# Kernel optimization log

Measured on AMD Instinct MI355X. Metric: run time of the kernel, lower is better.

Reference implementation:

```python
import jax, jax.numpy as jnp
import numpy as np

B, T, I, H, O = 64, 512, 256, 512, 256

def setup_inputs() -> dict:
    key = jax.random.key(0)
    ks = jax.random.split(key, 12)
    s = 1.0 / np.sqrt(H)
    u = lambda k, shp: jax.random.uniform(k, shp, jnp.float32, -s, s)
    return {
        'x': jax.random.normal(ks[0], (B, T, I), jnp.float32),
        'w_ih0': u(ks[1], (H, I)),  'w_hh0': u(ks[2], (H, H)),
        'b_ih0': u(ks[3], (H,)),    'b_hh0': u(ks[4], (H,)),
        'w_ih1': u(ks[5], (H, H)),  'w_hh1': u(ks[6], (H, H)),
        'b_ih1': u(ks[7], (H,)),    'b_hh1': u(ks[8], (H,)),
        'fc_w': u(ks[9], (O, H)),   'fc_b': u(ks[10], (O,)),
    }

def _rnn_layer(inp, w_ih, w_hh, b_ih, b_hh):
    # inp: [B, T, F] -> precompute input projection once (one big GEMM)
    xp = jnp.einsum('btf,hf->bth', inp, w_ih) + b_ih + b_hh  # [B, T, H]
    def step(h, xt):
        h = jnp.tanh(xt + h @ w_hh.T)  # [B, H]
        return h, h
    h0 = jnp.zeros((inp.shape[0], w_hh.shape[0]), inp.dtype)
    hT, outs = jax.lax.scan(step, h0, jnp.swapaxes(xp, 0, 1))  # outs: [T, B, H]
    return jnp.swapaxes(outs, 0, 1), hT

def reference(x, w_ih0, w_hh0, b_ih0, b_hh0, w_ih1, w_hh1, b_ih1, b_hh1, fc_w, fc_b):
    out0, h0f = _rnn_layer(x, w_ih0, w_hh0, b_ih0, b_hh0)
    out1, h1f = _rnn_layer(out0, w_ih1, w_hh1, b_ih1, b_hh1)
    hidden = jnp.stack([h0f, h1f])                  # [n_layers, B, H]
    out = out1.reshape(-1, out1.shape[-1]) @ fc_w.T + fc_b  # [B*T, O]
    return out, hidden
```

## Files before the change

### kernel.cpp

```cpp
#include <hip/hip_runtime.h>

#define B_  64
#define T_  512
#define I_  256
#define H_  512
#define O_  256
#define SENT 0x7F7F7F7Fu
#define SLOT_BYTES 8192u

typedef __attribute__((ext_vector_type(8))) __bf16 bf16x8;
typedef __attribute__((ext_vector_type(4))) float f32x4;
typedef unsigned int u32x4 __attribute__((ext_vector_type(4)));

__device__ __forceinline__ unsigned short f2bf(float f) {
    unsigned int u = __float_as_uint(f);
    unsigned int r = (u + 0x7fffu + ((u >> 16) & 1u)) >> 16;
    return (unsigned short)r;
}

__device__ __forceinline__ float tanh_fast(float x) {
    float e = __expf(2.0f * x);
    float d = e + 1.0f;
    float r;
    asm("v_rcp_f32 %0, %1" : "=v"(r) : "v"(d));
    return 1.0f - 2.0f * r;
}

__global__ void cvt_kernel(const float* __restrict__ in, unsigned short* __restrict__ out, int n4) {
    int i = blockIdx.x * blockDim.x + threadIdx.x;
    if (i >= n4) return;
    float4 f = reinterpret_cast<const float4*>(in)[i];
    ushort4 o;
    o.x = f2bf(f.x); o.y = f2bf(f.y); o.z = f2bf(f.z); o.w = f2bf(f.w);
    reinterpret_cast<ushort4*>(out)[i] = o;
}

__global__ __launch_bounds__(256) void gemm_kernel(
    const unsigned short* __restrict__ A,
    const unsigned short* __restrict__ Bw,
    const float* __restrict__ b0,
    const float* __restrict__ b1,
    float* __restrict__ C,
    int M, int N, int K, int perm)
{
    const int m0 = blockIdx.x * 64;
    const int n0 = blockIdx.y * 64;
    const int tid = threadIdx.x;
    const int wv = tid >> 6;
    const int l = tid & 63;
    const int lr = l & 15;
    const int lk = (l >> 4) * 8;
    const int arow = m0 + wv * 16 + lr;

    f32x4 acc[4] = {{0,0,0,0},{0,0,0,0},{0,0,0,0},{0,0,0,0}};
    const int nks = K / 32;
    for (int ks = 0; ks < nks; ++ks) {
        bf16x8 a = *reinterpret_cast<const bf16x8*>(A + (size_t)arow * K + ks * 32 + lk);
        #pragma unroll
        for (int nt = 0; nt < 4; ++nt) {
            bf16x8 b = *reinterpret_cast<const bf16x8*>(Bw + (size_t)(n0 + nt * 16 + lr) * K + ks * 32 + lk);
            acc[nt] = __builtin_amdgcn_mfma_f32_16x16x32_bf16(a, b, acc[nt], 0, 0, 0);
        }
    }
    #pragma unroll
    for (int nt = 0; nt < 4; ++nt) {
        #pragma unroll
        for (int r = 0; r < 4; ++r) {
            int row = m0 + wv * 16 + (l >> 4) * 4 + r;
            int col = n0 + nt * 16 + lr;
            float v = acc[nt][r];
            if (b0) v += b0[col];
            if (b1) v += b1[col];
            int cs = perm ? ((col & 15) * 32 + (col >> 4)) : col;
            C[(size_t)row * N + cs] = v;
        }
    }
}

#define LDW8(ARR, BASE) \
    asm volatile( \
        "global_load_dwordx4 %0, %8, %9 offset:0\n\t" \
        "global_load_dwordx4 %1, %8, %9 offset:64\n\t" \
        "global_load_dwordx4 %2, %8, %9 offset:128\n\t" \
        "global_load_dwordx4 %3, %8, %9 offset:192\n\t" \
        "global_load_dwordx4 %4, %8, %9 offset:256\n\t" \
        "global_load_dwordx4 %5, %8, %9 offset:320\n\t" \
        "global_load_dwordx4 %6, %8, %9 offset:384\n\t" \
        "global_load_dwordx4 %7, %8, %9 offset:448\n\t" \
        "s_waitcnt vmcnt(0)" \
        : "=&v"(ARR[0]), "=&v"(ARR[1]), "=&v"(ARR[2]), "=&v"(ARR[3]), \
          "=&v"(ARR[4]), "=&v"(ARR[5]), "=&v"(ARR[6]), "=&v"(ARR[7]) \
        : "v"(BASE), "s"(w))

#define LOAD_XP4(XPQ) \
    asm volatile( \
        "global_load_dwordx4 %0, %4, %8\n\t" \
        "global_load_dwordx4 %1, %5, %8\n\t" \
        "global_load_dwordx4 %2, %6, %8\n\t" \
        "global_load_dwordx4 %3, %7, %8\n\t" \
        "s_waitcnt vmcnt(0)" \
        : "=&v"(XPQ[0]), "=&v"(XPQ[1]), "=&v"(XPQ[2]), "=&v"(XPQ[3]) \
        : "v"(vxpr[0]), "v"(vxpr[1]), "v"(vxpr[2]), "v"(vxpr[3]), "s"(xpg))

#define ISSUE_XP4(XPQ) \
    asm volatile( \
        "global_load_dwordx4 %0, %4, %8\n\t" \
        "global_load_dwordx4 %1, %5, %8\n\t" \
        "global_load_dwordx4 %2, %6, %8\n\t" \
        "global_load_dwordx4 %3, %7, %8" \
        : "=&v"(XPQ[0]), "=&v"(XPQ[1]), "=&v"(XPQ[2]), "=&v"(XPQ[3]) \
        : "v"(vxpr[0]), "v"(vxpr[1]), "v"(vxpr[2]), "v"(vxpr[3]), "s"(xpg))

#define POLL8(AFP, VSLR, SC) \
    asm volatile( \
        "global_load_dwordx4 %0, %8, %9 " SC "\n\t" \
        "global_load_dwordx4 %1, %8, %9 offset:64 " SC "\n\t" \
        "global_load_dwordx4 %2, %8, %9 offset:128 " SC "\n\t" \
        "global_load_dwordx4 %3, %8, %9 offset:192 " SC "\n\t" \
        "global_load_dwordx4 %4, %8, %9 offset:256 " SC "\n\t" \
        "global_load_dwordx4 %5, %8, %9 offset:320 " SC "\n\t" \
        "global_load_dwordx4 %6, %8, %9 offset:384 " SC "\n\t" \
        "global_load_dwordx4 %7, %8, %9 offset:448 " SC "\n\t" \
        "s_waitcnt vmcnt(0)" \
        : "=&v"(AFP[0]), "=&v"(AFP[1]), "=&v"(AFP[2]), "=&v"(AFP[3]), \
          "=&v"(AFP[4]), "=&v"(AFP[5]), "=&v"(AFP[6]), "=&v"(AFP[7]) \
        : "v"(VSLR), "s"(slR))

#define SENT_CHECK(AFP, BAD) \
    { BAD = 0; \
      _Pragma("unroll") \
      for (int _i = 0; _i < 8; ++_i) \
          _Pragma("unroll") \
          for (int _j = 0; _j < 4; ++_j) \
              BAD |= (AFP[_i][_j] == SENT); }

#define STORE_SLOT16(PK, VSLW) \
    asm volatile( \
        "global_store_dword %16, %0, %17 sc0 sc1\n\t" \
        "global_store_dword %16, %1, %17 offset:512 sc0 sc1\n\t" \
        "global_store_dword %16, %2, %17 offset:1024 sc0 sc1\n\t" \
        "global_store_dword %16, %3, %17 offset:1536 sc0 sc1\n\t" \
        "global_store_dword %16, %4, %17 offset:32 sc0 sc1\n\t" \
        "global_store_dword %16, %5, %17 offset:544 sc0 sc1\n\t" \
        "global_store_dword %16, %6, %17 offset:1056 sc0 sc1\n\t" \
        "global_store_dword %16, %7, %17 offset:1568 sc0 sc1\n\t" \
        "global_store_dword %16, %8, %17 offset:64 sc0 sc1\n\t" \
        "global_store_dword %16, %9, %17 offset:576 sc0 sc1\n\t" \
        "global_store_dword %16, %10, %17 offset:1088 sc0 sc1\n\t" \
        "global_store_dword %16, %11, %17 offset:1600 sc0 sc1\n\t" \
        "global_store_dword %16, %12, %17 offset:96 sc0 sc1\n\t" \
        "global_store_dword %16, %13, %17 offset:608 sc0 sc1\n\t" \
        "global_store_dword %16, %14, %17 offset:1120 sc0 sc1\n\t" \
        "global_store_dword %16, %15, %17 offset:1632 sc0 sc1" \
        :: "v"(PK[0]), "v"(PK[1]), "v"(PK[2]), "v"(PK[3]), \
           "v"(PK[4]), "v"(PK[5]), "v"(PK[6]), "v"(PK[7]), \
           "v"(PK[8]), "v"(PK[9]), "v"(PK[10]), "v"(PK[11]), \
           "v"(PK[12]), "v"(PK[13]), "v"(PK[14]), "v"(PK[15]), \
           "v"(VSLW), "s"(slW) \
        : "memory")

#define OUT16(PK) \
    asm volatile( \
        "global_store_dword %16, %0, %20\n\t" \
        "global_store_dword %17, %1, %20\n\t" \
        "global_store_dword %18, %2, %20\n\t" \
        "global_store_dword %19, %3, %20\n\t" \
        "global_store_dword %16, %4, %20 offset:32\n\t" \
        "global_store_dword %17, %5, %20 offset:32\n\t" \
        "global_store_dword %18, %6, %20 offset:32\n\t" \
        "global_store_dword %19, %7, %20 offset:32\n\t" \
        "global_store_dword %16, %8, %20 offset:64\n\t" \
        "global_store_dword %17, %9, %20 offset:64\n\t" \
        "global_store_dword %18, %10, %20 offset:64\n\t" \
        "global_store_dword %19, %11, %20 offset:64\n\t" \
        "global_store_dword %16, %12, %20 offset:96\n\t" \
        "global_store_dword %17, %13, %20 offset:96\n\t" \
        "global_store_dword %18, %14, %20 offset:96\n\t" \
        "global_store_dword %19, %15, %20 offset:96" \
        :: "v"(PK[0]), "v"(PK[1]), "v"(PK[2]), "v"(PK[3]), \
           "v"(PK[4]), "v"(PK[5]), "v"(PK[6]), "v"(PK[7]), \
           "v"(PK[8]), "v"(PK[9]), "v"(PK[10]), "v"(PK[11]), \
           "v"(PK[12]), "v"(PK[13]), "v"(PK[14]), "v"(PK[15]), \
           "v"(vout[0]), "v"(vout[1]), "v"(vout[2]), "v"(vout[3]), \
           "s"(out_bf) \
        : "memory")

#define SENTRESET(VS) \
    asm volatile( \
        "global_store_dwordx4 %0, %1, %2 sc0 sc1\n\t" \
        "global_store_dwordx4 %0, %1, %2 offset:1024 sc0 sc1" \
        :: "v"(VS), "v"(sentq), "s"(slR) : "memory")

__global__ __launch_bounds__(256, 1) void recur_kernel(
    const float* __restrict__ xp,
    const unsigned short* __restrict__ w,
    unsigned short* __restrict__ out_bf,
    float* __restrict__ h_final,
    unsigned short* __restrict__ slots)
{
    __shared__ __align__(16) unsigned short lds[16 * 280];

    const int bid16 = blockIdx.x;
    if (bid16 & 4) return;
    const int g   = bid16 & 3;
    const int jw  = (bid16 >> 3) & 1;
    const int widx = g * 2 + jw;
    const int pjw = jw ^ 1;
    const int b0  = g * 16;
    const int tid = threadIdx.x;
    const int wv  = tid >> 6;
    const int l   = tid & 63;
    const int lr  = l & 15;
    const int lk  = (l >> 4) * 8;
    const int jn0 = jw * 256 + wv * 64;
    const int erow_l = (l >> 4) * 4;
    const int erow_g = b0 + erow_l;

    const float*          xpg = xp + (size_t)b0 * T_ * H_;
    float*                hfg = h_final + (size_t)b0 * H_;
    unsigned short*       slW = slots + (size_t)widx * 16384;
    const unsigned short* slR = slots + (size_t)(widx ^ 1) * 16384;

    bf16x8 bwo[4][8], bwp[4][8];
    #pragma unroll
    for (int nt = 0; nt < 4; ++nt) {
        unsigned int vo = (unsigned)((jn0 + nt * 16 + lr) * (H_ * 2) + jw  * 512 + lk * 2);
        unsigned int vp = (unsigned)((jn0 + nt * 16 + lr) * (H_ * 2) + pjw * 512 + lk * 2);
        LDW8(bwo[nt], vo);
        LDW8(bwp[nt], vp);
    }

    unsigned int vxpr[4], vout[4];
    #pragma unroll
    for (int r = 0; r < 4; ++r) {
        vxpr[r] = (unsigned)(((erow_l + r) * T_ * H_ + lr * 32 + jw * 16 + wv * 4) * 4);
        vout[r] = (unsigned)(((erow_g + r) * T_) * H_ * 2 + (jn0 + lr) * 2);
    }
    const unsigned int vslr0 = (unsigned)(lr * 512 + lk * 2);
    const unsigned int vslw0 = (unsigned)(erow_l * 512 + (wv * 64 + lr) * 2);
    const unsigned int vsent0 = (unsigned)(wv * 2048 + l * 16);
    const u32x4 sentq = {SENT, SENT, SENT, SENT};
    const int cb = wv * 32 + (lr >> 1);

    unsigned int pks[16];
    f32x4 xpq[4];

    {
        LOAD_XP4(xpq);
        #pragma unroll
        for (int nt = 0; nt < 4; ++nt)
            #pragma unroll
            for (int r = 0; r < 4; ++r) {
                float hv = tanh_fast(xpq[r][nt]);
                unsigned int mine = f2bf(hv);
                unsigned int oth = (unsigned int)__shfl_xor((int)mine, 1, 64);
                pks[nt * 4 + r] = mine | (oth << 16);
            }
        if (!(lr & 1)) {
            unsigned int* lw = (unsigned int*)lds;
            #pragma unroll
            for (int nt = 0; nt < 4; ++nt)
                #pragma unroll
                for (int r = 0; r < 4; ++r)
                    lw[(erow_l + r) * 140 + cb + nt * 8] = pks[nt * 4 + r];
            unsigned int vslw = vslw0 + 1u * SLOT_BYTES;
            STORE_SLOT16(pks, vslw);
        }
        #pragma unroll
        for (int r = 0; r < 4; ++r) vxpr[r] += H_ * 4;
        ISSUE_XP4(xpq);
        __syncthreads();
    }

    for (int t = 1; t < T_; ++t) {
        f32x4 acc[4] = {{0,0,0,0},{0,0,0,0},{0,0,0,0},{0,0,0,0}};
        {
            bf16x8 afo[8];
            const unsigned short* lrb = lds + lr * 280 + lk;
            #pragma unroll
            for (int i = 0; i < 8; ++i)
                afo[i] = *reinterpret_cast<const bf16x8*>(lrb + i * 32);
            #pragma unroll
            for (int i = 0; i < 8; ++i) {
                acc[0] = __builtin_amdgcn_mfma_f32_16x16x32_bf16(afo[i], bwo[0][i], acc[0], 0, 0, 0);
                acc[1] = __builtin_amdgcn_mfma_f32_16x16x32_bf16(afo[i], bwo[1][i], acc[1], 0, 0, 0);
                acc[2] = __builtin_amdgcn_mfma_f32_16x16x32_bf16(afo[i], bwo[2][i], acc[2], 0, 0, 0);
                acc[3] = __builtin_amdgcn_mfma_f32_16x16x32_bf16(afo[i], bwo[3][i], acc[3], 0, 0, 0);
            }
        }
        __syncthreads();

        const unsigned int vslr = vslr0 + (unsigned)(t & 3) * SLOT_BYTES;
        u32x4 afp[8];
        int bad;
        POLL8(afp, vslr, "sc0");
        SENT_CHECK(afp, bad);
        while (__any(bad)) {
            POLL8(afp, vslr, "sc0 sc1");
            SENT_CHECK(afp, bad);
            if (!__any(bad)) break;
            POLL8(afp, vslr, "sc0");
            SENT_CHECK(afp, bad);
        }
        __builtin_amdgcn_sched_barrier(0);

        if (!(lr & 1)) OUT16(pks);
        #pragma unroll
        for (int r = 0; r < 4; ++r) vout[r] += H_ * 2;

        #pragma unroll
        for (int i = 0; i < 8; ++i) {
            bf16x8 a = __builtin_bit_cast(bf16x8, afp[i]);
            acc[0] = __builtin_amdgcn_mfma_f32_16x16x32_bf16(a, bwp[0][i], acc[0], 0, 0, 0);
            acc[1] = __builtin_amdgcn_mfma_f32_16x16x32_bf16(a, bwp[1][i], acc[1], 0, 0, 0);
            acc[2] = __builtin_amdgcn_mfma_f32_16x16x32_bf16(a, bwp[2][i], acc[2], 0, 0, 0);
            acc[3] = __builtin_amdgcn_mfma_f32_16x16x32_bf16(a, bwp[3][i], acc[3], 0, 0, 0);
        }

        unsigned int pkn[16];
        #pragma unroll
        for (int nt = 0; nt < 4; ++nt)
            #pragma unroll
            for (int r = 0; r < 4; ++r) {
                float pre = acc[nt][r] + xpq[r][nt];
                float hv = tanh_fast(pre);
                if (t == T_ - 1)
                    hfg[(size_t)(erow_l + r) * H_ + jn0 + nt * 16 + lr] = hv;
                unsigned int mine = f2bf(hv);
                unsigned int oth = (unsigned int)__shfl_xor((int)mine, 1, 64);
                pkn[nt * 4 + r] = mine | (oth << 16);
            }
        if (!(lr & 1)) {
            unsigned int* lw = (unsigned int*)lds;
            #pragma unroll
            for (int nt = 0; nt < 4; ++nt)
                #pragma unroll
                for (int r = 0; r < 4; ++r)
                    lw[(erow_l + r) * 140 + cb + nt * 8] = pkn[nt * 4 + r];
            unsigned int vslw = vslw0 + (unsigned)((t + 1) & 3) * SLOT_BYTES;
            STORE_SLOT16(pkn, vslw);
        }
        #pragma unroll
        for (int r = 0; r < 4; ++r) vxpr[r] += H_ * 4;
        if (t < T_ - 1) ISSUE_XP4(xpq);
        #pragma unroll
        for (int i = 0; i < 16; ++i) pks[i] = pkn[i];

        __syncthreads();
        {
            unsigned int vs = vsent0 + (unsigned)(t & 3) * SLOT_BYTES;
            SENTRESET(vs);
        }
    }

    if (!(lr & 1)) OUT16(pks);
}

#define OFF_XBF    ((size_t)0)
#define OFF_WIH0   ((size_t)16777216)
#define OFF_WHH0   ((size_t)17039360)
#define OFF_WIH1   ((size_t)17563648)
#define OFF_WHH1   ((size_t)18087936)
#define OFF_FCW    ((size_t)18612224)
#define OFF_XP     ((size_t)18874368)
#define OFF_OUTBF  ((size_t)85983232)
#define OFF_SLOTS  ((size_t)119537664)
#define WS_NEED    ((size_t)119799808)

extern "C" void kernel_launch(void* const* d_in, const int* in_sizes, int n_in,
                              void* d_out, int out_size, void* d_ws, size_t ws_size,
                              hipStream_t stream) {
    if (ws_size < WS_NEED) return;
    const float* x     = (const float*)d_in[0];
    const float* w_ih0 = (const float*)d_in[1];
    const float* w_hh0 = (const float*)d_in[2];
    const float* b_ih0 = (const float*)d_in[3];
    const float* b_hh0 = (const float*)d_in[4];
    const float* w_ih1 = (const float*)d_in[5];
    const float* w_hh1 = (const float*)d_in[6];
    const float* b_ih1 = (const float*)d_in[7];
    const float* b_hh1 = (const float*)d_in[8];
    const float* fc_w  = (const float*)d_in[9];
    const float* fc_b  = (const float*)d_in[10];

    char* ws = (char*)d_ws;
    unsigned short* x_bf     = (unsigned short*)(ws + OFF_XBF);
    unsigned short* w_ih0_bf = (unsigned short*)(ws + OFF_WIH0);
    unsigned short* w_hh0_bf = (unsigned short*)(ws + OFF_WHH0);
    unsigned short* w_ih1_bf = (unsigned short*)(ws + OFF_WIH1);
    unsigned short* w_hh1_bf = (unsigned short*)(ws + OFF_WHH1);
    unsigned short* fc_w_bf  = (unsigned short*)(ws + OFF_FCW);
    float*          xp       = (float*)(ws + OFF_XP);
    unsigned short* out_bf   = (unsigned short*)(ws + OFF_OUTBF);
    unsigned short* slots    = (unsigned short*)(ws + OFF_SLOTS);

    float* out  = (float*)d_out;
    float* hid0 = out + (size_t)B_ * T_ * O_;
    float* hid1 = hid0 + (size_t)B_ * H_;

    hipMemsetAsync(ws + OFF_SLOTS, 0x7F, 262144, stream);

    auto cvt = [&](const float* in, unsigned short* o, int n) {
        int n4 = n / 4;
        cvt_kernel<<<(n4 + 255) / 256, 256, 0, stream>>>(in, o, n4);
    };
    cvt(x,     x_bf,     B_ * T_ * I_);
    cvt(w_ih0, w_ih0_bf, H_ * I_);
    cvt(w_hh0, w_hh0_bf, H_ * H_);
    cvt(w_ih1, w_ih1_bf, H_ * H_);
    cvt(w_hh1, w_hh1_bf, H_ * H_);
    cvt(fc_w,  fc_w_bf,  O_ * H_);

    const int M = B_ * T_;

    gemm_kernel<<<dim3(M / 64, H_ / 64), 256, 0, stream>>>(
        x_bf, w_ih0_bf, b_ih0, b_hh0, xp, M, H_, I_, 1);

    recur_kernel<<<16, 256, 0, stream>>>(xp, w_hh0_bf, out_bf, hid0, slots);

    gemm_kernel<<<dim3(M / 64, H_ / 64), 256, 0, stream>>>(
        out_bf, w_ih1_bf, b_ih1, b_hh1, xp, M, H_, H_, 1);

    hipMemsetAsync(ws + OFF_SLOTS, 0x7F, 262144, stream);

    recur_kernel<<<16, 256, 0, stream>>>(xp, w_hh1_bf, out_bf, hid1, slots);

    gemm_kernel<<<dim3(M / 64, O_ / 64), 256, 0, stream>>>(
        out_bf, fc_w_bf, fc_b, nullptr, out, M, O_, H_, 0);
}
```

Baseline: 4.307 ms.

## Process two batch groups per recurrent workgroup, halving workgroup count

Result: slower. 7.233 ms (+67.9%).

```diff
diff --git a/kernel.cpp b/kernel.cpp
--- a/kernel.cpp
+++ b/kernel.cpp
@@ -92,7 +92,7 @@
           "=&v"(ARR[4]), "=&v"(ARR[5]), "=&v"(ARR[6]), "=&v"(ARR[7]) \
         : "v"(BASE), "s"(w))
 
-#define LOAD_XP4(XPQ) \
+#define LOAD_XP4(XPQ, XPB) \
     asm volatile( \
         "global_load_dwordx4 %0, %4, %8\n\t" \
         "global_load_dwordx4 %1, %5, %8\n\t" \
@@ -100,41 +100,79 @@
         "global_load_dwordx4 %3, %7, %8\n\t" \
         "s_waitcnt vmcnt(0)" \
         : "=&v"(XPQ[0]), "=&v"(XPQ[1]), "=&v"(XPQ[2]), "=&v"(XPQ[3]) \
-        : "v"(vxpr[0]), "v"(vxpr[1]), "v"(vxpr[2]), "v"(vxpr[3]), "s"(xpg))
-
-#define ISSUE_XP4(XPQ) \
-    asm volatile( \
-        "global_load_dwordx4 %0, %4, %8\n\t" \
-        "global_load_dwordx4 %1, %5, %8\n\t" \
-        "global_load_dwordx4 %2, %6, %8\n\t" \
-        "global_load_dwordx4 %3, %7, %8" \
-        : "=&v"(XPQ[0]), "=&v"(XPQ[1]), "=&v"(XPQ[2]), "=&v"(XPQ[3]) \
-        : "v"(vxpr[0]), "v"(vxpr[1]), "v"(vxpr[2]), "v"(vxpr[3]), "s"(xpg))
-
-#define POLL8(AFP, VSLR, SC) \
-    asm volatile( \
-        "global_load_dwordx4 %0, %8, %9 " SC "\n\t" \
-        "global_load_dwordx4 %1, %8, %9 offset:64 " SC "\n\t" \
-        "global_load_dwordx4 %2, %8, %9 offset:128 " SC "\n\t" \
-        "global_load_dwordx4 %3, %8, %9 offset:192 " SC "\n\t" \
-        "global_load_dwordx4 %4, %8, %9 offset:256 " SC "\n\t" \
-        "global_load_dwordx4 %5, %8, %9 offset:320 " SC "\n\t" \
-        "global_load_dwordx4 %6, %8, %9 offset:384 " SC "\n\t" \
-        "global_load_dwordx4 %7, %8, %9 offset:448 " SC "\n\t" \
+        : "v"(vxpr[0]), "v"(vxpr[1]), "v"(vxpr[2]), "v"(vxpr[3]), "s"(XPB))
+
+#define LOAD2_XP_PEER() \
+    asm volatile( \
+        "global_load_dwordx4 %0, %24, %28\n\t" \
+        "global_load_dwordx4 %1, %25, %28\n\t" \
+        "global_load_dwordx4 %2, %26, %28\n\t" \
+        "global_load_dwordx4 %3, %27, %28\n\t" \
+        "global_load_dwordx4 %4, %24, %29\n\t" \
+        "global_load_dwordx4 %5, %25, %29\n\t" \
+        "global_load_dwordx4 %6, %26, %29\n\t" \
+        "global_load_dwordx4 %7, %27, %29\n\t" \
+        "global_load_dwordx4 %8, %30, %31 sc0 sc1\n\t" \
+        "global_load_dwordx4 %9, %30, %31 offset:64 sc0 sc1\n\t" \
+        "global_load_dwordx4 %10, %30, %31 offset:128 sc0 sc1\n\t" \
+        "global_load_dwordx4 %11, %30, %31 offset:192 sc0 sc1\n\t" \
+        "global_load_dwordx4 %12, %30, %31 offset:256 sc0 sc1\n\t" \
+        "global_load_dwordx4 %13, %30, %31 offset:320 sc0 sc1\n\t" \
+        "global_load_dwordx4 %14, %30, %31 offset:384 sc0 sc1\n\t" \
+        "global_load_dwordx4 %15, %30, %31 offset:448 sc0 sc1\n\t" \
+        "global_load_dwordx4 %16, %30, %32 sc0 sc1\n\t" \
+        "global_load_dwordx4 %17, %30, %32 offset:64 sc0 sc1\n\t" \
+        "global_load_dwordx4 %18, %30, %32 offset:128 sc0 sc1\n\t" \
+        "global_load_dwordx4 %19, %30, %32 offset:192 sc0 sc1\n\t" \
+        "global_load_dwordx4 %20, %30, %32 offset:256 sc0 sc1\n\t" \
+        "global_load_dwordx4 %21, %30, %32 offset:320 sc0 sc1\n\t" \
+        "global_load_dwordx4 %22, %30, %32 offset:384 sc0 sc1\n\t" \
+        "global_load_dwordx4 %23, %30, %32 offset:448 sc0 sc1\n\t" \
         "s_waitcnt vmcnt(0)" \
-        : "=&v"(AFP[0]), "=&v"(AFP[1]), "=&v"(AFP[2]), "=&v"(AFP[3]), \
-          "=&v"(AFP[4]), "=&v"(AFP[5]), "=&v"(AFP[6]), "=&v"(AFP[7]) \
-        : "v"(VSLR), "s"(slR))
-
-#define SENT_CHECK(AFP, BAD) \
+        : "=&v"(xpqA[0]), "=&v"(xpqA[1]), "=&v"(xpqA[2]), "=&v"(xpqA[3]), \
+          "=&v"(xpqB[0]), "=&v"(xpqB[1]), "=&v"(xpqB[2]), "=&v"(xpqB[3]), \
+          "=&v"(afpA[0]), "=&v"(afpA[1]), "=&v"(afpA[2]), "=&v"(afpA[3]), \
+          "=&v"(afpA[4]), "=&v"(afpA[5]), "=&v"(afpA[6]), "=&v"(afpA[7]), \
+          "=&v"(afpB[0]), "=&v"(afpB[1]), "=&v"(afpB[2]), "=&v"(afpB[3]), \
+          "=&v"(afpB[4]), "=&v"(afpB[5]), "=&v"(afpB[6]), "=&v"(afpB[7]) \
+        : "v"(vxpr[0]), "v"(vxpr[1]), "v"(vxpr[2]), "v"(vxpr[3]), \
+          "s"(xpA), "s"(xpB), "v"(vslr), "s"(slRA), "s"(slRB))
+
+#define RETRY16() \
+    asm volatile( \
+        "global_load_dwordx4 %0, %16, %17 sc0 sc1\n\t" \
+        "global_load_dwordx4 %1, %16, %17 offset:64 sc0 sc1\n\t" \
+        "global_load_dwordx4 %2, %16, %17 offset:128 sc0 sc1\n\t" \
+        "global_load_dwordx4 %3, %16, %17 offset:192 sc0 sc1\n\t" \
+        "global_load_dwordx4 %4, %16, %17 offset:256 sc0 sc1\n\t" \
+        "global_load_dwordx4 %5, %16, %17 offset:320 sc0 sc1\n\t" \
+        "global_load_dwordx4 %6, %16, %17 offset:384 sc0 sc1\n\t" \
+        "global_load_dwordx4 %7, %16, %17 offset:448 sc0 sc1\n\t" \
+        "global_load_dwordx4 %8, %16, %18 sc0 sc1\n\t" \
+        "global_load_dwordx4 %9, %16, %18 offset:64 sc0 sc1\n\t" \
+        "global_load_dwordx4 %10, %16, %18 offset:128 sc0 sc1\n\t" \
+        "global_load_dwordx4 %11, %16, %18 offset:192 sc0 sc1\n\t" \
+        "global_load_dwordx4 %12, %16, %18 offset:256 sc0 sc1\n\t" \
+        "global_load_dwordx4 %13, %16, %18 offset:320 sc0 sc1\n\t" \
+        "global_load_dwordx4 %14, %16, %18 offset:384 sc0 sc1\n\t" \
+        "global_load_dwordx4 %15, %16, %18 offset:448 sc0 sc1\n\t" \
+        "s_waitcnt vmcnt(0)" \
+        : "=&v"(afpA[0]), "=&v"(afpA[1]), "=&v"(afpA[2]), "=&v"(afpA[3]), \
+          "=&v"(afpA[4]), "=&v"(afpA[5]), "=&v"(afpA[6]), "=&v"(afpA[7]), \
+          "=&v"(afpB[0]), "=&v"(afpB[1]), "=&v"(afpB[2]), "=&v"(afpB[3]), \
+          "=&v"(afpB[4]), "=&v"(afpB[5]), "=&v"(afpB[6]), "=&v"(afpB[7]) \
+        : "v"(vslr), "s"(slRA), "s"(slRB))
+
+#define SENT_CHECK2(BAD) \
     { BAD = 0; \
       _Pragma("unroll") \
       for (int _i = 0; _i < 8; ++_i) \
           _Pragma("unroll") \
-          for (int _j = 0; _j < 4; ++_j) \
-              BAD |= (AFP[_i][_j] == SENT); }
-
-#define STORE_SLOT16(PK, VSLW) \
+          for (int _j = 0; _j < 4; ++_j) { \
+              BAD |= (afpA[_i][_j] == SENT); \
+              BAD |= (afpB[_i][_j] == SENT); } }
+
+#define STORE_SLOT16(PK, VSLW, SLWB) \
     asm volatile( \
         "global_store_dword %16, %0, %17 sc0 sc1\n\t" \
         "global_store_dword %16, %1, %17 offset:512 sc0 sc1\n\t" \
@@ -156,10 +194,10 @@
            "v"(PK[4]), "v"(PK[5]), "v"(PK[6]), "v"(PK[7]), \
            "v"(PK[8]), "v"(PK[9]), "v"(PK[10]), "v"(PK[11]), \
            "v"(PK[12]), "v"(PK[13]), "v"(PK[14]), "v"(PK[15]), \
-           "v"(VSLW), "s"(slW) \
+           "v"(VSLW), "s"(SLWB) \
         : "memory")
 
-#define OUT16(PK) \
+#define OUT16(PK, OUTB) \
     asm volatile( \
         "global_store_dword %16, %0, %20\n\t" \
         "global_store_dword %17, %1, %20\n\t" \
@@ -182,14 +220,14 @@
            "v"(PK[8]), "v"(PK[9]), "v"(PK[10]), "v"(PK[11]), \
            "v"(PK[12]), "v"(PK[13]), "v"(PK[14]), "v"(PK[15]), \
            "v"(vout[0]), "v"(vout[1]), "v"(vout[2]), "v"(vout[3]), \
-           "s"(out_bf) \
+           "s"(OUTB) \
         : "memory")
 
-#define SENTRESET(VS) \
+#define SENTRESET(VS, SLRB) \
     asm volatile( \
         "global_store_dwordx4 %0, %1, %2 sc0 sc1\n\t" \
         "global_store_dwordx4 %0, %1, %2 offset:1024 sc0 sc1" \
-        :: "v"(VS), "v"(sentq), "s"(slR) : "memory")
+        :: "v"(VS), "v"(sentq), "s"(SLRB) : "memory")
 
 __global__ __launch_bounds__(256, 1) void recur_kernel(
     const float* __restrict__ xp,
@@ -198,15 +236,14 @@
     float* __restrict__ h_final,
     unsigned short* __restrict__ slots)
 {
-    __shared__ __align__(16) unsigned short lds[16 * 280];
-
-    const int bid16 = blockIdx.x;
-    if (bid16 & 4) return;
-    const int g   = bid16 & 3;
-    const int jw  = (bid16 >> 3) & 1;
-    const int widx = g * 2 + jw;
+    __shared__ __align__(16) unsigned short lds[32 * 280];
+
+    const int bid = blockIdx.x;
+    const int gp  = bid >> 1;
+    const int jw  = bid & 1;
     const int pjw = jw ^ 1;
-    const int b0  = g * 16;
+    const int gA  = gp;
+    const int gB  = gp + 2;
     const int tid = threadIdx.x;
     const int wv  = tid >> 6;
     const int l   = tid & 63;
@@ -214,12 +251,17 @@
     const int lk  = (l >> 4) * 8;
     const int jn0 = jw * 256 + wv * 64;
     const int erow_l = (l >> 4) * 4;
-    const int erow_g = b0 + erow_l;
-
-    const float*          xpg = xp + (size_t)b0 * T_ * H_;
-    float*                hfg = h_final + (size_t)b0 * H_;
-    unsigned short*       slW = slots + (size_t)widx * 16384;
-    const unsigned short* slR = slots + (size_t)(widx ^ 1) * 16384;
+
+    const float*          xpA  = xp + (size_t)(gA * 16) * T_ * H_;
+    const float*          xpB  = xp + (size_t)(gB * 16) * T_ * H_;
+    unsigned short*       outA = out_bf + (size_t)(gA * 16) * T_ * H_;
+    unsigned short*       outB = out_bf + (size_t)(gB * 16) * T_ * H_;
+    float*                hfA  = h_final + (size_t)(gA * 16) * H_;
+    float*                hfB  = h_final + (size_t)(gB * 16) * H_;
+    unsigned short*       slWA = slots + (size_t)(gA * 2 + jw) * 16384;
+    unsigned short*       slWB = slots + (size_t)(gB * 2 + jw) * 16384;
+    const unsigned short* slRA = slots + (size_t)(gA * 2 + pjw) * 16384;
+    const unsigned short* slRB = slots + (size_t)(gB * 2 + pjw) * 16384;
 
     bf16x8 bwo[4][8], bwp[4][8];
     #pragma unroll
@@ -234,7 +276,7 @@
     #pragma unroll
     for (int r = 0; r < 4; ++r) {
         vxpr[r] = (unsigned)(((erow_l + r) * T_ * H_ + lr * 32 + jw * 16 + wv * 4) * 4);
-        vout[r] = (unsigned)(((erow_g + r) * T_) * H_ * 2 + (jn0 + lr) * 2);
+        vout[r] = (unsigned)(((erow_l + r) * T_) * H_ * 2 + (jn0 + lr) * 2);
     }
     const unsigned int vslr0 = (unsigned)(lr * 512 + lk * 2);
     const unsigned int vslw0 = (unsigned)(erow_l * 512 + (wv * 64 + lr) * 2);
@@ -242,38 +284,41 @@
     const u32x4 sentq = {SENT, SENT, SENT, SENT};
     const int cb = wv * 32 + (lr >> 1);
 
-    unsigned int pks[16];
-    f32x4 xpq[4];
-
     {
-        LOAD_XP4(xpq);
-        #pragma unroll
-        for (int nt = 0; nt < 4; ++nt)
-            #pragma unroll
-            for (int r = 0; r < 4; ++r) {
-                float hv = tanh_fast(xpq[r][nt]);
-                unsigned int mine = f2bf(hv);
-                unsigned int oth = (unsigned int)__shfl_xor((int)mine, 1, 64);
-                pks[nt * 4 + r] = mine | (oth << 16);
-            }
-        if (!(lr & 1)) {
-            unsigned int* lw = (unsigned int*)lds;
+        #pragma unroll
+        for (int grp = 0; grp < 2; ++grp) {
+            f32x4 xpq[4];
+            if (grp == 0) { LOAD_XP4(xpq, xpA); } else { LOAD_XP4(xpq, xpB); }
+            unsigned int pk[16];
             #pragma unroll
             for (int nt = 0; nt < 4; ++nt)
                 #pragma unroll
-                for (int r = 0; r < 4; ++r)
-                    lw[(erow_l + r) * 140 + cb + nt * 8] = pks[nt * 4 + r];
-            unsigned int vslw = vslw0 + 1u * SLOT_BYTES;
-            STORE_SLOT16(pks, vslw);
-        }
-        #pragma unroll
-        for (int r = 0; r < 4; ++r) vxpr[r] += H_ * 4;
-        ISSUE_XP4(xpq);
+                for (int r = 0; r < 4; ++r) {
+                    float hv = tanh_fast(xpq[r][nt]);
+                    unsigned int mine = f2bf(hv);
+                    unsigned int oth = (unsigned int)__shfl_xor((int)mine, 1, 64);
+                    pk[nt * 4 + r] = mine | (oth << 16);
+                }
+            if (!(lr & 1)) {
+                unsigned int* lw = (unsigned int*)lds;
+                #pragma unroll
+                for (int nt = 0; nt < 4; ++nt)
+                    #pragma unroll
+                    for (int r = 0; r < 4; ++r)
+                        lw[(grp * 16 + erow_l + r) * 140 + cb + nt * 8] = pk[nt * 4 + r];
+                unsigned int vslw = vslw0 + 1u * SLOT_BYTES;
+                if (grp == 0) { STORE_SLOT16(pk, vslw, slWA); OUT16(pk, outA); }
+                else          { STORE_SLOT16(pk, vslw, slWB); OUT16(pk, outB); }
+            }
+        }
         __syncthreads();
+        #pragma unroll
+        for (int r = 0; r < 4; ++r) { vxpr[r] += H_ * 4; vout[r] += H_ * 2; }
     }
 
     for (int t = 1; t < T_; ++t) {
-        f32x4 acc[4] = {{0,0,0,0},{0,0,0,0},{0,0,0,0},{0,0,0,0}};
+        f32x4 accA[4] = {{0,0,0,0},{0,0,0,0},{0,0,0,0},{0,0,0,0}};
+        f32x4 accB[4] = {{0,0,0,0},{0,0,0,0},{0,0,0,0},{0,0,0,0}};
         {
             bf16x8 afo[8];
             const unsigned short* lrb = lds + lr * 280 + lk;
@@ -282,78 +327,95 @@
                 afo[i] = *reinterpret_cast<const bf16x8*>(lrb + i * 32);
             #pragma unroll
             for (int i = 0; i < 8; ++i) {
-                acc[0] = __builtin_amdgcn_mfma_f32_16x16x32_bf16(afo[i], bwo[0][i], acc[0], 0, 0, 0);
-                acc[1] = __builtin_amdgcn_mfma_f32_16x16x32_bf16(afo[i], bwo[1][i], acc[1], 0, 0, 0);
-                acc[2] = __builtin_amdgcn_mfma_f32_16x16x32_bf16(afo[i], bwo[2][i], acc[2], 0, 0, 0);
-                acc[3] = __builtin_amdgcn_mfma_f32_16x16x32_bf16(afo[i], bwo[3][i], acc[3], 0, 0, 0);
+                accA[0] = __builtin_amdgcn_mfma_f32_16x16x32_bf16(afo[i], bwo[0][i], accA[0], 0, 0, 0);
+                accA[1] = __builtin_amdgcn_mfma_f32_16x16x32_bf16(afo[i], bwo[1][i], accA[1], 0, 0, 0);
+                accA[2] = __builtin_amdgcn_mfma_f32_16x16x32_bf16(afo[i], bwo[2][i], accA[2], 0, 0, 0);
+                accA[3] = __builtin_amdgcn_mfma_f32_16x16x32_bf16(afo[i], bwo[3][i], accA[3], 0, 0, 0);
             }
         }
+        {
+            bf16x8 afo[8];
+            const unsigned short* lrb = lds + (16 + lr) * 280 + lk;
+            #pragma unroll
+            for (int i = 0; i < 8; ++i)
+                afo[i] = *reinterpret_cast<const bf16x8*>(lrb + i * 32);
+            #pragma unroll
+            for (int i = 0; i < 8; ++i) {
+                accB[0] = __builtin_amdgcn_mfma_f32_16x16x32_bf16(afo[i], bwo[0][i], accB[0], 0, 0, 0);
+                accB[1] = __builtin_amdgcn_mfma_f32_16x16x32_bf16(afo[i], bwo[1][i], accB[1], 0, 0, 0);
+                accB[2] = __builtin_amdgcn_mfma_f32_16x16x32_bf16(afo[i], bwo[2][i], accB[2], 0, 0, 0);
+                accB[3] = __builtin_amdgcn_mfma_f32_16x16x32_bf16(afo[i], bwo[3][i], accB[3], 0, 0, 0);
+            }
+        }
         __syncthreads();
 
         const unsigned int vslr = vslr0 + (unsigned)(t & 3) * SLOT_BYTES;
-        u32x4 afp[8];
+        f32x4 xpqA[4], xpqB[4];
+        u32x4 afpA[8], afpB[8];
+        LOAD2_XP_PEER();
         int bad;
-        POLL8(afp, vslr, "sc0");
-        SENT_CHECK(afp, bad);
-        while (__any(bad)) {
-            POLL8(afp, vslr, "sc0 sc1");
-            SENT_CHECK(afp, bad);
-            if (!__any(bad)) break;
-            POLL8(afp, vslr, "sc0");
-            SENT_CHECK(afp, bad);
-        }
+        SENT_CHECK2(bad);
+        while (__any(bad)) { RETRY16(); SENT_CHECK2(bad); }
         __builtin_amdgcn_sched_barrier(0);
 
-        if (!(lr & 1)) OUT16(pks);
-        #pragma unroll
-        for (int r = 0; r < 4; ++r) vout[r] += H_ * 2;
-
         #pragma unroll
         for (int i = 0; i < 8; ++i) {
-            bf16x8 a = __builtin_bit_cast(bf16x8, afp[i]);
-            acc[0] = __builtin_amdgcn_mfma_f32_16x16x32_bf16(a, bwp[0][i], acc[0], 0, 0, 0);
-            acc[1] = __builtin_amdgcn_mfma_f32_16x16x32_bf16(a, bwp[1][i], acc[1], 0, 0, 0);
-            acc[2] = __builtin_amdgcn_mfma_f32_16x16x32_bf16(a, bwp[2][i], acc[2], 0, 0, 0);
-            acc[3] = __builtin_amdgcn_mfma_f32_16x16x32_bf16(a, bwp[3][i], acc[3], 0, 0, 0);
-        }
-
-        unsigned int pkn[16];
-        #pragma unroll
-        for (int nt = 0; nt < 4; ++nt)
-            #pragma unroll
-            for (int r = 0; r < 4; ++r) {
-                float pre = acc[nt][r] + xpq[r][nt];
-                float hv = tanh_fast(pre);
-                if (t == T_ - 1)
-                    hfg[(size_t)(erow_l + r) * H_ + jn0 + nt * 16 + lr] = hv;
-                unsigned int mine = f2bf(hv);
-                unsigned int oth = (unsigned int)__shfl_xor((int)mine, 1, 64);
-                pkn[nt * 4 + r] = mine | (oth << 16);
-            }
-        if (!(lr & 1)) {
-            unsigned int* lw = (unsigned int*)lds;
+            bf16x8 a = __builtin_bit_cast(bf16x8, afpA[i]);
+            accA[0] = __builtin_amdgcn_mfma_f32_16x16x32_bf16(a, bwp[0][i], accA[0], 0, 0, 0);
+            accA[1] = __builtin_amdgcn_mfma_f32_16x16x32_bf16(a, bwp[1][i], accA[1], 0, 0, 0);
+            accA[2] = __builtin_amdgcn_mfma_f32_16x16x32_bf16(a, bwp[2][i], accA[2], 0, 0, 0);
+            accA[3] = __builtin_amdgcn_mfma_f32_16x16x32_bf16(a, bwp[3][i], accA[3], 0, 0, 0);
+        }
+        #pragma unroll
+        for (int i = 0; i < 8; ++i) {
+            bf16x8 a = __builtin_bit_cast(bf16x8, afpB[i]);
+            accB[0] = __builtin_amdgcn_mfma_f32_16x16x32_bf16(a, bwp[0][i], accB[0], 0, 0, 0);
+            accB[1] = __builtin_amdgcn_mfma_f32_16x16x32_bf16(a, bwp[1][i], accB[1], 0, 0, 0);
+            accB[2] = __builtin_amdgcn_mfma_f32_16x16x32_bf16(a, bwp[2][i], accB[2], 0, 0, 0);
+            accB[3] = __builtin_amdgcn_mfma_f32_16x16x32_bf16(a, bwp[3][i], accB[3], 0, 0, 0);
+        }
+
+        #pragma unroll
+        for (int grp = 0; grp < 2; ++grp) {
+            f32x4* acc = grp ? accB : accA;
+            f32x4* xpq = grp ? xpqB : xpqA;
+            unsigned int pk[16];
             #pragma unroll
             for (int nt = 0; nt < 4; ++nt)
                 #pragma unroll
-                for (int r = 0; r < 4; ++r)
-                    lw[(erow_l + r) * 140 + cb + nt * 8] = pkn[nt * 4 + r];
-            unsigned int vslw = vslw0 + (unsigned)((t + 1) & 3) * SLOT_BYTES;
-            STORE_SLOT16(pkn, vslw);
-        }
-        #pragma unroll
-        for (int r = 0; r < 4; ++r) vxpr[r] += H_ * 4;
-        if (t < T_ - 1) ISSUE_XP4(xpq);
-        #pragma unroll
-        for (int i = 0; i < 16; ++i) pks[i] = pkn[i];
+                for (int r = 0; r < 4; ++r) {
+                    float pre = acc[nt][r] + xpq[r][nt];
+                    float hv = tanh_fast(pre);
+                    if (t == T_ - 1) {
+                        float* hfg = grp ? hfB : hfA;
+                        hfg[(size_t)(erow_l + r) * H_ + jn0 + nt * 16 + lr] = hv;
+                    }
+                    unsigned int mine = f2bf(hv);
+                    unsigned int oth = (unsigned int)__shfl_xor((int)mine, 1, 64);
+                    pk[nt * 4 + r] = mine | (oth << 16);
+                }
+            if (!(lr & 1)) {
+                unsigned int* lw = (unsigned int*)lds;
+                #pragma unroll
+                for (int nt = 0; nt < 4; ++nt)
+                    #pragma unroll
+                    for (int r = 0; r < 4; ++r)
+                        lw[(grp * 16 + erow_l + r) * 140 + cb + nt * 8] = pk[nt * 4 + r];
+                unsigned int vslw = vslw0 + (unsigned)((t + 1) & 3) * SLOT_BYTES;
+                if (grp == 0) { STORE_SLOT16(pk, vslw, slWA); OUT16(pk, outA); }
+                else          { STORE_SLOT16(pk, vslw, slWB); OUT16(pk, outB); }
+            }
+        }
 
         __syncthreads();
         {
             unsigned int vs = vsent0 + (unsigned)(t & 3) * SLOT_BYTES;
-            SENTRESET(vs);
-        }
-    }
-
-    if (!(lr & 1)) OUT16(pks);
+            SENTRESET(vs, slRA);
+            SENTRESET(vs, slRB);
+        }
+        #pragma unroll
+        for (int r = 0; r < 4; ++r) { vxpr[r] += H_ * 4; vout[r] += H_ * 2; }
+    }
 }
 
 #define OFF_XBF    ((size_t)0)
@@ -416,14 +478,14 @@
     gemm_kernel<<<dim3(M / 64, H_ / 64), 256, 0, stream>>>(
         x_bf, w_ih0_bf, b_ih0, b_hh0, xp, M, H_, I_, 1);
 
-    recur_kernel<<<16, 256, 0, stream>>>(xp, w_hh0_bf, out_bf, hid0, slots);
+    recur_kernel<<<4, 256, 0, stream>>>(xp, w_hh0_bf, out_bf, hid0, slots);
 
     gemm_kernel<<<dim3(M / 64, H_ / 64), 256, 0, stream>>>(
         out_bf, w_ih1_bf, b_ih1, b_hh1, xp, M, H_, H_, 1);
 
     hipMemsetAsync(ws + OFF_SLOTS, 0x7F, 262144, stream);
 
-    recur_kernel<<<16, 256, 0, stream>>>(xp, w_hh1_bf, out_bf, hid1, slots);
+    recur_kernel<<<4, 256, 0, stream>>>(xp, w_hh1_bf, out_bf, hid1, slots);
 
     gemm_kernel<<<dim3(M / 64, O_ / 64), 256, 0, stream>>>(
         out_bf, fc_w_bf, fc_b, nullptr, out, M, O_, H_, 0);
```
